# Kernel optimization log

Hardware: AMD Instinct MI355X
Metric: run time of the kernel (lower is better)

The kernel has to match this reference:

```python
import jax, jax.numpy as jnp
import numpy as np

B, L, D, F_, H = 64, 64, 512, 32, 512  # batch, seq_len, in_dim, fanout, hidden_dim


def setup_inputs() -> dict:
    key = jax.random.key(0)
    ks = jax.random.split(key, 8)
    x = jax.random.normal(ks[0], (B, L, D), dtype=jnp.float32)
    idx1 = jax.random.randint(ks[1], (B, F_), 0, L)          # hop-1 neighbor token ids
    idx2 = jax.random.randint(ks[2], (B, F_ * F_), 0, L)     # hop-2 neighbor token ids
    s_d = 1.0 / np.sqrt(D)
    s_h = 1.0 / np.sqrt(H)
    W_aggr0 = jax.random.normal(ks[3], (D, H), dtype=jnp.float32) * s_d
    b_aggr0 = jnp.zeros((H,), dtype=jnp.float32)
    W_self0 = jax.random.normal(ks[4], (D, H), dtype=jnp.float32) * s_d
    W_aggr1 = jax.random.normal(ks[5], (H, H), dtype=jnp.float32) * s_h
    b_aggr1 = jnp.zeros((H,), dtype=jnp.float32)
    W_self1 = jax.random.normal(ks[6], (H, H), dtype=jnp.float32) * s_h
    return {"x": x, "idx1": idx1, "idx2": idx2,
            "W_aggr0": W_aggr0, "b_aggr0": b_aggr0, "W_self0": W_self0,
            "W_aggr1": W_aggr1, "b_aggr1": b_aggr1, "W_self1": W_self1}


def _sage_gcn(src, nbr, W_aggr, b_aggr, W_self):
    # src: [B, N, d]; nbr: [B, N, F, d]. mean-aggregate + linear, sum with self-transform.
    aggr = jnp.mean(nbr, axis=2) @ W_aggr + b_aggr          # NeighborAggregator('mean')
    return src @ W_self + aggr                               # aggr_hidden_method='sum'


def reference(x, idx1, idx2, W_aggr0, b_aggr0, W_self0, W_aggr1, b_aggr1, W_self1):
    # Gather sampled node features per aspect (level 0 = aspect node itself, index 0).
    f0 = x[:, :1, :]                                               # [B, 1, D]
    f1 = jnp.take_along_axis(x, idx1[:, :, None], axis=1)          # [B, F, D]
    f2 = jnp.take_along_axis(x, idx2[:, :, None], axis=1)          # [B, F*F, D]

    # Layer 0 (shared gcn[0] weights across hops), leaky_relu activation.
    h0 = jax.nn.leaky_relu(_sage_gcn(f0, f1[:, None, :, :], W_aggr0, b_aggr0, W_self0))          # [B,1,H]
    h1 = jax.nn.leaky_relu(_sage_gcn(f1, f2.reshape(B, F_, F_, D), W_aggr0, b_aggr0, W_self0))   # [B,F,H]

    # Layer 1 (gcn[-1], activation=None).
    out = _sage_gcn(h0, h1[:, None, :, :], W_aggr1, b_aggr1, W_self1)                             # [B,1,H]
    return out
```

## Files before the change

kernel.cpp:

```cpp
#include <hip/hip_runtime.h>
#include <hip/hip_bf16.h>

#define B_ 64
#define L_ 64
#define D_ 512
#define F_ 32
#define H_ 512
#define M_ROWS 2048
#define M2 2112
#define KA 1024

typedef __attribute__((ext_vector_type(8))) short bf16x8;
typedef __attribute__((ext_vector_type(4))) float f32x4;

__device__ __forceinline__ float leaky(float v) { return v > 0.0f ? v : 0.01f * v; }

__device__ __forceinline__ unsigned short f2bf(float v) {
  unsigned int b = __float_as_uint(v);
  unsigned int r = b + 0x7FFF + ((b >> 16) & 1);
  return (unsigned short)(r >> 16);
}
__device__ __forceinline__ float bf2f(unsigned short h) {
  return __uint_as_float(((unsigned int)h) << 16);
}
__device__ __forceinline__ void cvt_store4(unsigned short* ph, unsigned short* pl, float4 v) {
  ushort4 h, l;
  h.x = f2bf(v.x); l.x = f2bf(v.x - bf2f(h.x));
  h.y = f2bf(v.y); l.y = f2bf(v.y - bf2f(h.y));
  h.z = f2bf(v.z); l.z = f2bf(v.z - bf2f(h.z));
  h.w = f2bf(v.w); l.w = f2bf(v.w - bf2f(h.w));
  *(ushort4*)ph = h;
  *(ushort4*)pl = l;
}

#define GLOAD16(GP, LP)                                              \
  __builtin_amdgcn_global_load_lds(                                  \
      (const __attribute__((address_space(1))) unsigned int*)(GP),   \
      (__attribute__((address_space(3))) unsigned int*)(LP), 16, 0, 0)

__global__ __launch_bounds__(256) void prep(
    const float* __restrict__ x, const int* __restrict__ idx1,
    const int* __restrict__ idx2,
    const float* __restrict__ Ws0, const float* __restrict__ Wa0,
    const float* __restrict__ Ws1, const float* __restrict__ Wa1,
    unsigned short* __restrict__ Xhi, unsigned short* __restrict__ Xlo,
    unsigned short* __restrict__ Mh, unsigned short* __restrict__ Ml,
    unsigned short* __restrict__ W0thi, unsigned short* __restrict__ W0tlo,
    unsigned short* __restrict__ W1thi, unsigned short* __restrict__ W1tlo) {
  __shared__ __align__(16) char smem[33024];
  const int blk = blockIdx.x;
  const int t = threadIdx.x;

  if (blk < 64) {
    const int b = blk;
    const float* src = x + (size_t)b * (L_ * D_);
    unsigned short* dh = Xhi + (size_t)b * (L_ * D_);
    unsigned short* dl = Xlo + (size_t)b * (L_ * D_);
#pragma unroll 4
    for (int i = 0; i < 32; ++i) {
      const int f4 = t + 256 * i;
      const float4 v = *(const float4*)(src + (size_t)f4 * 4);
      cvt_store4(dh + (size_t)f4 * 4, dl + (size_t)f4 * 4, v);
    }
  } else if (blk < 320) {
    const int q = blk - 64;
    const int k0 = (q & 15) * 64;
    const int n0 = ((q >> 4) & 7) * 64;
    const int cat = q >> 7;
    float (*lt)[72] = (float(*)[72])smem;
    const float* src = (cat == 0)
        ? (k0 < 512 ? Ws0 + (size_t)k0 * H_ : Wa0 + (size_t)(k0 - 512) * H_)
        : (k0 < 512 ? Ws1 + (size_t)k0 * H_ : Wa1 + (size_t)(k0 - 512) * H_);
    unsigned short* dhi = (cat == 0) ? W0thi : W1thi;
    unsigned short* dlo = (cat == 0) ? W0tlo : W1tlo;
#pragma unroll
    for (int i = 0; i < 4; ++i) {
      const int idx4 = t + 256 * i;
      const int kl = idx4 >> 4;
      const int n4 = (idx4 & 15) * 4;
      *(float4*)&lt[kl][n4] = *(const float4*)(src + (size_t)kl * H_ + n0 + n4);
    }
    __syncthreads();
#pragma unroll
    for (int i = 0; i < 4; ++i) {
      const int idx4 = t + 256 * i;
      const int nl = idx4 >> 4;
      const int k4 = (idx4 & 15) * 4;
      ushort4 h, l;
      const float v0 = lt[k4 + 0][nl], v1 = lt[k4 + 1][nl];
      const float v2 = lt[k4 + 2][nl], v3 = lt[k4 + 3][nl];
      h.x = f2bf(v0); l.x = f2bf(v0 - bf2f(h.x));
      h.y = f2bf(v1); l.y = f2bf(v1 - bf2f(h.y));
      h.z = f2bf(v2); l.z = f2bf(v2 - bf2f(h.z));
      h.w = f2bf(v3); l.w = f2bf(v3 - bf2f(h.w));
      *(ushort4*)(dhi + (size_t)(n0 + nl) * KA + k0 + k4) = h;
      *(ushort4*)(dlo + (size_t)(n0 + nl) * KA + k0 + k4) = l;
    }
  } else {
    const int q = blk - 320;
    const int b = q >> 2;
    const int nt0 = (q & 3) * 2;
    unsigned int* cnt = (unsigned int*)smem;
    unsigned short* Cm = (unsigned short*)(smem + 8448);
    unsigned short* XTh = (unsigned short*)(smem + 14592);
    unsigned short* XTl = XTh + 64 * 72;
    const int lane = t & 63;
    const int w = t >> 6;
    const int lr = lane & 15;
    const int kb8 = (lane >> 4) * 8;

#pragma unroll
    for (int i = 0; i < 9; ++i) { const int p = t + 256 * i; if (p < 2112) cnt[p] = 0u; }
#pragma unroll
    for (int i = 0; i < 12; ++i) Cm[t + 256 * i] = 0;
    __syncthreads();
#pragma unroll
    for (int i = 0; i < 4; ++i) {
      const int j = t + 256 * i;
      atomicAdd(&cnt[(j >> 5) * 64 + idx2[(size_t)b * 1024 + j]], 1u);
    }
    if (t < 32) atomicAdd(&cnt[32 * 64 + idx1[b * F_ + t]], 1u);
    __syncthreads();
#pragma unroll
    for (int i = 0; i < 9; ++i) {
      const int p = t + 256 * i;
      if (p < 2112) Cm[p] = f2bf((float)cnt[p] * 0.03125f);
    }
    __syncthreads();
    bf16x8 Af[3][2];
#pragma unroll
    for (int mi = 0; mi < 3; ++mi)
#pragma unroll
      for (int kt = 0; kt < 2; ++kt)
        Af[mi][kt] = *(const bf16x8*)&Cm[(mi * 16 + lr) * 64 + kt * 32 + kb8];

#pragma unroll
    for (int tt = 0; tt < 2; ++tt) {
      const int nbase = (nt0 + tt) * 64;
#pragma unroll
      for (int i = 0; i < 4; ++i) {
        const int f4 = t + 256 * i;
        const int l = f4 >> 4;
        const int c4 = (f4 & 15) * 4;
        const float4 v = *(const float4*)(x + (size_t)b * (L_ * D_) + (size_t)l * D_ + nbase + c4);
        unsigned short h;
        h = f2bf(v.x); XTh[(c4 + 0) * 72 + l] = h; XTl[(c4 + 0) * 72 + l] = f2bf(v.x - bf2f(h));
        h = f2bf(v.y); XTh[(c4 + 1) * 72 + l] = h; XTl[(c4 + 1) * 72 + l] = f2bf(v.y - bf2f(h));
        h = f2bf(v.z); XTh[(c4 + 2) * 72 + l] = h; XTl[(c4 + 2) * 72 + l] = f2bf(v.z - bf2f(h));
        h = f2bf(v.w); XTh[(c4 + 3) * 72 + l] = h; XTl[(c4 + 3) * 72 + l] = f2bf(v.w - bf2f(h));
      }
      __syncthreads();
      f32x4 acc[3] = {};
#pragma unroll
      for (int kt = 0; kt < 2; ++kt) {
        const bf16x8 Bh = *(const bf16x8*)&XTh[(w * 16 + lr) * 72 + kt * 32 + kb8];
        const bf16x8 Bl = *(const bf16x8*)&XTl[(w * 16 + lr) * 72 + kt * 32 + kb8];
#pragma unroll
        for (int mi = 0; mi < 3; ++mi) {
          acc[mi] = __builtin_amdgcn_mfma_f32_16x16x32_bf16(Af[mi][kt], Bh, acc[mi], 0, 0, 0);
          acc[mi] = __builtin_amdgcn_mfma_f32_16x16x32_bf16(Af[mi][kt], Bl, acc[mi], 0, 0, 0);
        }
      }
      const int col = nbase + w * 16 + lr;
#pragma unroll
      for (int mi = 0; mi < 3; ++mi)
#pragma unroll
        for (int r = 0; r < 4; ++r) {
          const int row48 = mi * 16 + (lane >> 4) * 4 + r;
          if (row48 > 32) continue;
          const size_t Mrow = (row48 < 32) ? (size_t)(b * F_ + row48) : (size_t)(M_ROWS + b);
          const float v = acc[mi][r];
          const unsigned short h = f2bf(v);
          Mh[Mrow * 512 + col] = h;
          Ml[Mrow * 512 + col] = f2bf(v - bf2f(h));
        }
      __syncthreads();
    }
  }
}

__global__ __launch_bounds__(256) void gemm1(
    const unsigned short* __restrict__ Xhi, const unsigned short* __restrict__ Xlo,
    const unsigned short* __restrict__ Mh, const unsigned short* __restrict__ Ml,
    const unsigned short* __restrict__ Wthi, const unsigned short* __restrict__ Wtlo,
    const int* __restrict__ idx1, const float* __restrict__ b0,
    unsigned short* __restrict__ Hhi, unsigned short* __restrict__ Hlo) {
  __shared__ unsigned short lds[24576];
  const int tid = threadIdx.x;
  const int lane = tid & 63;
  const int w = tid >> 6;
  const int wr = w >> 1, wc = w & 1;
  const int lr = lane & 15;
  const int kb = lane >> 4;
  const int swz = lr & 7;
  const int rsel = lane >> 3;
  const int cbs = ((lane & 7) ^ rsel) * 8;

  const int o = blockIdx.x;
  const int s = (o & 7) * 66 + (o >> 3);
  const int bmi = s >> 4;
  const int bni = s & 15;
  const int bm = bmi * 64;
  const int bn = bni * 32;

  int xrow[8];
  if (w < 2) {
#pragma unroll
    for (int i = 0; i < 8; ++i) {
      const int R = bm + rsel + 8 * i;
      if (bmi < 32) xrow[i] = (R >> 5) * 64 + idx1[R];
      else          xrow[i] = (R - M_ROWS) * 64;
    }
  }
  const unsigned short* Xp = (w == 0) ? Xhi : Xlo;
  const unsigned short* Mp = (w == 0) ? Mh : Ml;
  const unsigned short* Wp = (w == 2) ? Wthi : Wtlo;
  const unsigned short* mbase = Mp + (size_t)(bm + rsel) * 512 + cbs;
  const unsigned short* wbase = Wp + (size_t)(bn + rsel) * KA + cbs;
  const int PB = (w == 0) ? 0 : (w == 1) ? 4096 : (w == 2) ? 8192 : 10240;

#define STAGE(KT, BUF)                                                        \
  {                                                                           \
    unsigned short* ldst = &lds[(BUF)*12288 + PB];                            \
    if (w < 2) {                                                              \
      if ((KT) < 8) {                                                         \
        const int co = (KT)*64 + cbs;                                         \
        _Pragma("unroll") for (int i = 0; i < 8; ++i)                         \
            GLOAD16(Xp + (size_t)xrow[i] * 512 + co, ldst + i * 512);         \
      } else {                                                                \
        const unsigned short* mb = mbase + ((KT)-8) * 64;                     \
        _Pragma("unroll") for (int i = 0; i < 8; ++i)                         \
            GLOAD16(mb + (size_t)i * 8 * 512, ldst + i * 512);                \
      }                                                                       \
    } else {                                                                  \
      const unsigned short* wb = wbase + (KT)*64;                             \
      _Pragma("unroll") for (int i = 0; i < 4; ++i)                           \
          GLOAD16(wb + (size_t)i * 8 * KA, ldst + i * 512);                   \
    }                                                                         \
  }

  f32x4 acc[2] = {};
  STAGE(0, 0);
  __syncthreads();

#define AFRAG(PL, ROW, CB) \
  (*(const bf16x8*)&lds[buf * 12288 + (PL)*4096 + (ROW)*64 + (((CB) ^ swz) * 8)])
#define BFRAG(PL, ROW, CB) \
  (*(const bf16x8*)&lds[buf * 12288 + 8192 + (PL)*2048 + (ROW)*64 + (((CB) ^ swz) * 8)])

  for (int kt = 0; kt < 16; ++kt) {
    const int buf = kt & 1;
    if (kt < 15) STAGE(kt + 1, buf ^ 1);
#pragma unroll
    for (int ks = 0; ks < 2; ++ks) {
      const int c = ks * 4 + kb;
      const bf16x8 Ah0 = AFRAG(0, wr * 32 + lr, c);
      const bf16x8 Ah1 = AFRAG(0, wr * 32 + 16 + lr, c);
      const bf16x8 Al0 = AFRAG(1, wr * 32 + lr, c);
      const bf16x8 Al1 = AFRAG(1, wr * 32 + 16 + lr, c);
      const bf16x8 Bh = BFRAG(0, wc * 16 + lr, c);
      const bf16x8 Bl = BFRAG(1, wc * 16 + lr, c);
      acc[0] = __builtin_amdgcn_mfma_f32_16x16x32_bf16(Ah0, Bh, acc[0], 0, 0, 0);
      acc[0] = __builtin_amdgcn_mfma_f32_16x16x32_bf16(Ah0, Bl, acc[0], 0, 0, 0);
      acc[0] = __builtin_amdgcn_mfma_f32_16x16x32_bf16(Al0, Bh, acc[0], 0, 0, 0);
      acc[1] = __builtin_amdgcn_mfma_f32_16x16x32_bf16(Ah1, Bh, acc[1], 0, 0, 0);
      acc[1] = __builtin_amdgcn_mfma_f32_16x16x32_bf16(Ah1, Bl, acc[1], 0, 0, 0);
      acc[1] = __builtin_amdgcn_mfma_f32_16x16x32_bf16(Al1, Bh, acc[1], 0, 0, 0);
    }
    __syncthreads();
  }
#undef AFRAG
#undef BFRAG
#undef STAGE

  const int col = bn + wc * 16 + lr;
  const float bias = b0[col];
  if (bmi < 32) {
    const int b = bmi * 2 + wr;
    float sum = 0.f;
#pragma unroll
    for (int mi = 0; mi < 2; ++mi)
#pragma unroll
      for (int r = 0; r < 4; ++r) sum += leaky(acc[mi][r] + bias);
    sum += __shfl_xor(sum, 16);
    sum += __shfl_xor(sum, 32);
    sum *= (1.0f / 32.0f);
    if (lane < 16) {
      const unsigned short h = f2bf(sum);
      Hhi[(size_t)b * KA + 512 + col] = h;
      Hlo[(size_t)b * KA + 512 + col] = f2bf(sum - bf2f(h));
    }
  } else {
#pragma unroll
    for (int mi = 0; mi < 2; ++mi)
#pragma unroll
      for (int r = 0; r < 4; ++r) {
        const int b = wr * 32 + mi * 16 + kb * 4 + r;
        const float v = leaky(acc[mi][r] + bias);
        const unsigned short h = f2bf(v);
        Hhi[(size_t)b * KA + col] = h;
        Hlo[(size_t)b * KA + col] = f2bf(v - bf2f(h));
      }
  }
}

__global__ __launch_bounds__(256) void gemm2(
    const unsigned short* __restrict__ Hhi, const unsigned short* __restrict__ Hlo,
    const unsigned short* __restrict__ Wthi, const unsigned short* __restrict__ Wtlo,
    float* __restrict__ part) {
  __shared__ float sacc[256][17];
  const int tid = threadIdx.x;
  const int w = tid >> 6;
  const int lane = tid & 63;
  const int lr = lane & 15;
  const int kb = lane >> 4;
  const int n0 = blockIdx.x * 16;
  const int kc = blockIdx.y * 128;

  f32x4 acc[4] = {};
  const int k = kc + w * 32 + kb * 8;
  const bf16x8 Bh = *(const bf16x8*)(Wthi + (size_t)(n0 + lr) * KA + k);
  const bf16x8 Bl = *(const bf16x8*)(Wtlo + (size_t)(n0 + lr) * KA + k);
#pragma unroll
  for (int mi = 0; mi < 4; ++mi) {
    const bf16x8 Ah = *(const bf16x8*)(Hhi + (size_t)(mi * 16 + lr) * KA + k);
    const bf16x8 Al = *(const bf16x8*)(Hlo + (size_t)(mi * 16 + lr) * KA + k);
    acc[mi] = __builtin_amdgcn_mfma_f32_16x16x32_bf16(Ah, Bh, acc[mi], 0, 0, 0);
    acc[mi] = __builtin_amdgcn_mfma_f32_16x16x32_bf16(Ah, Bl, acc[mi], 0, 0, 0);
    acc[mi] = __builtin_amdgcn_mfma_f32_16x16x32_bf16(Al, Bh, acc[mi], 0, 0, 0);
  }
#pragma unroll
  for (int mi = 0; mi < 4; ++mi)
#pragma unroll
    for (int r = 0; r < 4; ++r)
      sacc[((w * 4 + mi) * 4 + kb) * 4 + r][lr] = acc[mi][r];
  __syncthreads();

  const int lr2 = tid & 15;
  const int rg = tid >> 4;
  float* pp = part + (size_t)blockIdx.y * (B_ * H_);
#pragma unroll
  for (int q = 0; q < 4; ++q) {
    const int row = rg * 4 + q;
    const int mi = row >> 4, kb2 = (row >> 2) & 3, r = row & 3;
    float s = 0.f;
#pragma unroll
    for (int w2 = 0; w2 < 4; ++w2)
      s += sacc[((w2 * 4 + mi) * 4 + kb2) * 4 + r][lr2];
    pp[(size_t)row * H_ + n0 + lr2] = s;
  }
}

__global__ __launch_bounds__(256) void reduce_out(
    const float* __restrict__ part, const float* __restrict__ b1,
    float* __restrict__ out) {
  const int idx = blockIdx.x * 256 + threadIdx.x;
  const int c4 = (idx & 127) * 4;
  const size_t off = (size_t)(idx >> 7) * H_ + c4;
  float4 s = *(const float4*)(b1 + c4);
#pragma unroll
  for (int ky = 0; ky < 8; ++ky) {
    const float4 p = *(const float4*)(part + (size_t)ky * (B_ * H_) + off);
    s.x += p.x; s.y += p.y; s.z += p.z; s.w += p.w;
  }
  *(float4*)(out + off) = s;
}

extern "C" void kernel_launch(void* const* d_in, const int* in_sizes, int n_in,
                              void* d_out, int out_size, void* d_ws, size_t ws_size,
                              hipStream_t stream) {
  const float* x    = (const float*)d_in[0];
  const int*   idx1 = (const int*)d_in[1];
  const int*   idx2 = (const int*)d_in[2];
  const float* Wa0  = (const float*)d_in[3];
  const float* b0   = (const float*)d_in[4];
  const float* Ws0  = (const float*)d_in[5];
  const float* Wa1  = (const float*)d_in[6];
  const float* b1   = (const float*)d_in[7];
  const float* Ws1  = (const float*)d_in[8];
  float* out = (float*)d_out;

  unsigned short* wsu = (unsigned short*)d_ws;
  unsigned short* Xhi   = wsu;
  unsigned short* Xlo   = Xhi + (size_t)4096 * 512;
  unsigned short* Mh    = Xlo + (size_t)4096 * 512;
  unsigned short* Ml    = Mh + (size_t)M2 * 512;
  unsigned short* W0thi = Ml + (size_t)M2 * 512;
  unsigned short* W0tlo = W0thi + (size_t)H_ * KA;
  unsigned short* W1thi = W0tlo + (size_t)H_ * KA;
  unsigned short* W1tlo = W1thi + (size_t)H_ * KA;
  unsigned short* Hhi   = W1tlo + (size_t)H_ * KA;
  unsigned short* Hlo   = Hhi + (size_t)B_ * KA;
  float* part = (float*)(Hlo + (size_t)B_ * KA);

  prep<<<576, 256, 0, stream>>>(x, idx1, idx2, Ws0, Wa0, Ws1, Wa1,
                                Xhi, Xlo, Mh, Ml, W0thi, W0tlo, W1thi, W1tlo);
  gemm1<<<528, 256, 0, stream>>>(Xhi, Xlo, Mh, Ml, W0thi, W0tlo,
                                 idx1, b0, Hhi, Hlo);
  gemm2<<<dim3(32, 8), 256, 0, stream>>>(Hhi, Hlo, W1thi, W1tlo, part);
  reduce_out<<<32, 256, 0, stream>>>(part, b1, out);
}
```

Measured before the change: 40.64 us.

## Restructure gemm1: stage weights in LDS per half, stream A directly from global

```diff
diff --git a/kernel.cpp b/kernel.cpp
--- a/kernel.cpp
+++ b/kernel.cpp
@@ -185,16 +185,12 @@
     const unsigned short* __restrict__ Wthi, const unsigned short* __restrict__ Wtlo,
     const int* __restrict__ idx1, const float* __restrict__ b0,
     unsigned short* __restrict__ Hhi, unsigned short* __restrict__ Hlo) {
-  __shared__ unsigned short lds[24576];
+  __shared__ __align__(16) unsigned short lds[32768];
   const int tid = threadIdx.x;
   const int lane = tid & 63;
   const int w = tid >> 6;
-  const int wr = w >> 1, wc = w & 1;
   const int lr = lane & 15;
-  const int kb = lane >> 4;
-  const int swz = lr & 7;
-  const int rsel = lane >> 3;
-  const int cbs = ((lane & 7) ^ rsel) * 8;
+  const int kq = lane >> 4;
 
   const int o = blockIdx.x;
   const int s = (o & 7) * 66 + (o >> 3);
@@ -203,104 +199,96 @@
   const int bm = bmi * 64;
   const int bn = bni * 32;
 
-  int xrow[8];
-  if (w < 2) {
-#pragma unroll
-    for (int i = 0; i < 8; ++i) {
-      const int R = bm + rsel + 8 * i;
-      if (bmi < 32) xrow[i] = (R >> 5) * 64 + idx1[R];
-      else          xrow[i] = (R - M_ROWS) * 64;
-    }
-  }
-  const unsigned short* Xp = (w == 0) ? Xhi : Xlo;
-  const unsigned short* Mp = (w == 0) ? Mh : Ml;
-  const unsigned short* Wp = (w == 2) ? Wthi : Wtlo;
-  const unsigned short* mbase = Mp + (size_t)(bm + rsel) * 512 + cbs;
-  const unsigned short* wbase = Wp + (size_t)(bn + rsel) * KA + cbs;
-  const int PB = (w == 0) ? 0 : (w == 1) ? 4096 : (w == 2) ? 8192 : 10240;
-
-#define STAGE(KT, BUF)                                                        \
-  {                                                                           \
-    unsigned short* ldst = &lds[(BUF)*12288 + PB];                            \
-    if (w < 2) {                                                              \
-      if ((KT) < 8) {                                                         \
-        const int co = (KT)*64 + cbs;                                         \
-        _Pragma("unroll") for (int i = 0; i < 8; ++i)                         \
-            GLOAD16(Xp + (size_t)xrow[i] * 512 + co, ldst + i * 512);         \
-      } else {                                                                \
-        const unsigned short* mb = mbase + ((KT)-8) * 64;                     \
-        _Pragma("unroll") for (int i = 0; i < 8; ++i)                         \
-            GLOAD16(mb + (size_t)i * 8 * 512, ldst + i * 512);                \
-      }                                                                       \
-    } else {                                                                  \
-      const unsigned short* wb = wbase + (KT)*64;                             \
-      _Pragma("unroll") for (int i = 0; i < 4; ++i)                           \
-          GLOAD16(wb + (size_t)i * 8 * KA, ldst + i * 512);                   \
-    }                                                                         \
-  }
-
-  f32x4 acc[2] = {};
-  STAGE(0, 0);
-  __syncthreads();
-
-#define AFRAG(PL, ROW, CB) \
-  (*(const bf16x8*)&lds[buf * 12288 + (PL)*4096 + (ROW)*64 + (((CB) ^ swz) * 8)])
-#define BFRAG(PL, ROW, CB) \
-  (*(const bf16x8*)&lds[buf * 12288 + 8192 + (PL)*2048 + (ROW)*64 + (((CB) ^ swz) * 8)])
-
-  for (int kt = 0; kt < 16; ++kt) {
-    const int buf = kt & 1;
-    if (kt < 15) STAGE(kt + 1, buf ^ 1);
-#pragma unroll
-    for (int ks = 0; ks < 2; ++ks) {
-      const int c = ks * 4 + kb;
-      const bf16x8 Ah0 = AFRAG(0, wr * 32 + lr, c);
-      const bf16x8 Ah1 = AFRAG(0, wr * 32 + 16 + lr, c);
-      const bf16x8 Al0 = AFRAG(1, wr * 32 + lr, c);
-      const bf16x8 Al1 = AFRAG(1, wr * 32 + 16 + lr, c);
-      const bf16x8 Bh = BFRAG(0, wc * 16 + lr, c);
-      const bf16x8 Bl = BFRAG(1, wc * 16 + lr, c);
-      acc[0] = __builtin_amdgcn_mfma_f32_16x16x32_bf16(Ah0, Bh, acc[0], 0, 0, 0);
-      acc[0] = __builtin_amdgcn_mfma_f32_16x16x32_bf16(Ah0, Bl, acc[0], 0, 0, 0);
-      acc[0] = __builtin_amdgcn_mfma_f32_16x16x32_bf16(Al0, Bh, acc[0], 0, 0, 0);
-      acc[1] = __builtin_amdgcn_mfma_f32_16x16x32_bf16(Ah1, Bh, acc[1], 0, 0, 0);
-      acc[1] = __builtin_amdgcn_mfma_f32_16x16x32_bf16(Ah1, Bl, acc[1], 0, 0, 0);
-      acc[1] = __builtin_amdgcn_mfma_f32_16x16x32_bf16(Al1, Bh, acc[1], 0, 0, 0);
-    }
-    __syncthreads();
-  }
-#undef AFRAG
-#undef BFRAG
-#undef STAGE
-
-  const int col = bn + wc * 16 + lr;
-  const float bias = b0[col];
+  const int R = bm + w * 16 + lr;
+  const int xr = (bmi < 32) ? ((R >> 5) * 64 + idx1[R]) : ((R - M_ROWS) * 64);
+  const unsigned short* aXh = Xhi + (size_t)xr * 512 + kq * 8;
+  const unsigned short* aXl = Xlo + (size_t)xr * 512 + kq * 8;
+  const unsigned short* aMh = Mh + (size_t)R * 512 + kq * 8;
+  const unsigned short* aMl = Ml + (size_t)R * 512 + kq * 8;
+
+  f32x4 accHH[2] = {};
+  f32x4 accX[2] = {};
+
+  for (int c = 0; c < 2; ++c) {
+#pragma unroll
+    for (int i = 0; i < 16; ++i) {
+      const int slot = (w * 16 + i) * 64 + lane;
+      const int pl = slot >> 11;
+      const int row = (slot >> 6) & 31;
+      const int cb = slot & 63;
+      const unsigned short* gp = (pl ? Wtlo : Wthi) +
+          (size_t)(bn + row) * KA + c * 512 + ((cb ^ (row & 7)) * 8);
+      GLOAD16(gp, &lds[(w * 16 + i) * 512]);
+    }
+    __syncthreads();
+
+    const unsigned short* ah = (c == 0) ? aXh : aMh;
+    const unsigned short* al = (c == 0) ? aXl : aMl;
+
+    bf16x8 Ah = *(const bf16x8*)(ah);
+    bf16x8 Al = *(const bf16x8*)(al);
+#pragma unroll
+    for (int ks = 0; ks < 16; ++ks) {
+      const int nk = (ks + 1) & 15;
+      const bf16x8 AhN = *(const bf16x8*)(ah + nk * 32);
+      const bf16x8 AlN = *(const bf16x8*)(al + nk * 32);
+#pragma unroll
+      for (int nf = 0; nf < 2; ++nf) {
+        const int row = nf * 16 + lr;
+        const int cbX = (ks * 4 + kq) ^ (row & 7);
+        const bf16x8 Bh = *(const bf16x8*)&lds[row * 512 + cbX * 8];
+        const bf16x8 Bl = *(const bf16x8*)&lds[16384 + row * 512 + cbX * 8];
+        accHH[nf] = __builtin_amdgcn_mfma_f32_16x16x32_bf16(Ah, Bh, accHH[nf], 0, 0, 0);
+        accX[nf]  = __builtin_amdgcn_mfma_f32_16x16x32_bf16(Ah, Bl, accX[nf], 0, 0, 0);
+        accX[nf]  = __builtin_amdgcn_mfma_f32_16x16x32_bf16(Al, Bh, accX[nf], 0, 0, 0);
+      }
+      Ah = AhN;
+      Al = AlN;
+    }
+    __syncthreads();
+  }
+
+  f32x4 acc[2];
+  acc[0] = accHH[0] + accX[0];
+  acc[1] = accHH[1] + accX[1];
+
   if (bmi < 32) {
-    const int b = bmi * 2 + wr;
-    float sum = 0.f;
-#pragma unroll
-    for (int mi = 0; mi < 2; ++mi)
-#pragma unroll
-      for (int r = 0; r < 4; ++r) sum += leaky(acc[mi][r] + bias);
-    sum += __shfl_xor(sum, 16);
-    sum += __shfl_xor(sum, 32);
-    sum *= (1.0f / 32.0f);
-    if (lane < 16) {
-      const unsigned short h = f2bf(sum);
-      Hhi[(size_t)b * KA + 512 + col] = h;
-      Hlo[(size_t)b * KA + 512 + col] = f2bf(sum - bf2f(h));
+    float* P = (float*)lds;
+#pragma unroll
+    for (int nf = 0; nf < 2; ++nf) {
+      const int col = bn + nf * 16 + lr;
+      const float bias = b0[col];
+      float sv = 0.f;
+#pragma unroll
+      for (int r = 0; r < 4; ++r) sv += leaky(acc[nf][r] + bias);
+      sv += __shfl_xor(sv, 16);
+      sv += __shfl_xor(sv, 32);
+      if (lane < 16) P[w * 32 + nf * 16 + lane] = sv;
+    }
+    __syncthreads();
+    if (tid < 64) {
+      const int half = tid >> 5;
+      const int col = tid & 31;
+      const int b = bmi * 2 + half;
+      const float sv = (P[(half * 2) * 32 + col] + P[(half * 2 + 1) * 32 + col]) * (1.0f / 32.0f);
+      const unsigned short h = f2bf(sv);
+      Hhi[(size_t)b * KA + 512 + bn + col] = h;
+      Hlo[(size_t)b * KA + 512 + bn + col] = f2bf(sv - bf2f(h));
     }
   } else {
 #pragma unroll
-    for (int mi = 0; mi < 2; ++mi)
+    for (int nf = 0; nf < 2; ++nf) {
+      const int col = bn + nf * 16 + lr;
+      const float bias = b0[col];
 #pragma unroll
       for (int r = 0; r < 4; ++r) {
-        const int b = wr * 32 + mi * 16 + kb * 4 + r;
-        const float v = leaky(acc[mi][r] + bias);
+        const int bb = w * 16 + kq * 4 + r;
+        const float v = leaky(acc[nf][r] + bias);
         const unsigned short h = f2bf(v);
-        Hhi[(size_t)b * KA + col] = h;
-        Hlo[(size_t)b * KA + col] = f2bf(v - bf2f(h));
+        Hhi[(size_t)bb * KA + col] = h;
+        Hlo[(size_t)bb * KA + col] = f2bf(v - bf2f(h));
       }
+    }
   }
 }
 
@@ -343,11 +331,11 @@
   for (int q = 0; q < 4; ++q) {
     const int row = rg * 4 + q;
     const int mi = row >> 4, kb2 = (row >> 2) & 3, r = row & 3;
-    float s = 0.f;
+    float sv = 0.f;
 #pragma unroll
     for (int w2 = 0; w2 < 4; ++w2)
-      s += sacc[((w2 * 4 + mi) * 4 + kb2) * 4 + r][lr2];
-    pp[(size_t)row * H_ + n0 + lr2] = s;
+      sv += sacc[((w2 * 4 + mi) * 4 + kb2) * 4 + r][lr2];
+    pp[(size_t)row * H_ + n0 + lr2] = sv;
   }
 }
 
```

After: 56.86 us. 1.4x slower.

## Fuse split-K reduction and bias into single-block-per-column gemm2

Applied to the files above, without the earlier changes.

```diff
diff --git a/kernel.cpp b/kernel.cpp
--- a/kernel.cpp
+++ b/kernel.cpp
@@ -304,66 +304,51 @@
   }
 }
 
-__global__ __launch_bounds__(256) void gemm2(
+__global__ __launch_bounds__(512) void gemm2f(
     const unsigned short* __restrict__ Hhi, const unsigned short* __restrict__ Hlo,
     const unsigned short* __restrict__ Wthi, const unsigned short* __restrict__ Wtlo,
-    float* __restrict__ part) {
-  __shared__ float sacc[256][17];
+    const float* __restrict__ b1, float* __restrict__ out) {
+  __shared__ float sacc[8][1088];
   const int tid = threadIdx.x;
   const int w = tid >> 6;
   const int lane = tid & 63;
   const int lr = lane & 15;
   const int kb = lane >> 4;
   const int n0 = blockIdx.x * 16;
-  const int kc = blockIdx.y * 128;
+  const int kc = w * 128;
 
   f32x4 acc[4] = {};
-  const int k = kc + w * 32 + kb * 8;
-  const bf16x8 Bh = *(const bf16x8*)(Wthi + (size_t)(n0 + lr) * KA + k);
-  const bf16x8 Bl = *(const bf16x8*)(Wtlo + (size_t)(n0 + lr) * KA + k);
-#pragma unroll
-  for (int mi = 0; mi < 4; ++mi) {
-    const bf16x8 Ah = *(const bf16x8*)(Hhi + (size_t)(mi * 16 + lr) * KA + k);
-    const bf16x8 Al = *(const bf16x8*)(Hlo + (size_t)(mi * 16 + lr) * KA + k);
-    acc[mi] = __builtin_amdgcn_mfma_f32_16x16x32_bf16(Ah, Bh, acc[mi], 0, 0, 0);
-    acc[mi] = __builtin_amdgcn_mfma_f32_16x16x32_bf16(Ah, Bl, acc[mi], 0, 0, 0);
-    acc[mi] = __builtin_amdgcn_mfma_f32_16x16x32_bf16(Al, Bh, acc[mi], 0, 0, 0);
+#pragma unroll
+  for (int ks = 0; ks < 4; ++ks) {
+    const int k = kc + ks * 32 + kb * 8;
+    const bf16x8 Bh = *(const bf16x8*)(Wthi + (size_t)(n0 + lr) * KA + k);
+    const bf16x8 Bl = *(const bf16x8*)(Wtlo + (size_t)(n0 + lr) * KA + k);
+#pragma unroll
+    for (int mi = 0; mi < 4; ++mi) {
+      const bf16x8 Ah = *(const bf16x8*)(Hhi + (size_t)(mi * 16 + lr) * KA + k);
+      const bf16x8 Al = *(const bf16x8*)(Hlo + (size_t)(mi * 16 + lr) * KA + k);
+      acc[mi] = __builtin_amdgcn_mfma_f32_16x16x32_bf16(Ah, Bh, acc[mi], 0, 0, 0);
+      acc[mi] = __builtin_amdgcn_mfma_f32_16x16x32_bf16(Ah, Bl, acc[mi], 0, 0, 0);
+      acc[mi] = __builtin_amdgcn_mfma_f32_16x16x32_bf16(Al, Bh, acc[mi], 0, 0, 0);
+    }
   }
 #pragma unroll
   for (int mi = 0; mi < 4; ++mi)
 #pragma unroll
     for (int r = 0; r < 4; ++r)
-      sacc[((w * 4 + mi) * 4 + kb) * 4 + r][lr] = acc[mi][r];
+      sacc[w][(mi * 16 + kb * 4 + r) * 17 + lr] = acc[mi][r];
   __syncthreads();
 
-  const int lr2 = tid & 15;
-  const int rg = tid >> 4;
-  float* pp = part + (size_t)blockIdx.y * (B_ * H_);
-#pragma unroll
-  for (int q = 0; q < 4; ++q) {
-    const int row = rg * 4 + q;
-    const int mi = row >> 4, kb2 = (row >> 2) & 3, r = row & 3;
-    float s = 0.f;
-#pragma unroll
-    for (int w2 = 0; w2 < 4; ++w2)
-      s += sacc[((w2 * 4 + mi) * 4 + kb2) * 4 + r][lr2];
-    pp[(size_t)row * H_ + n0 + lr2] = s;
-  }
-}
-
-__global__ __launch_bounds__(256) void reduce_out(
-    const float* __restrict__ part, const float* __restrict__ b1,
-    float* __restrict__ out) {
-  const int idx = blockIdx.x * 256 + threadIdx.x;
-  const int c4 = (idx & 127) * 4;
-  const size_t off = (size_t)(idx >> 7) * H_ + c4;
-  float4 s = *(const float4*)(b1 + c4);
-#pragma unroll
-  for (int ky = 0; ky < 8; ++ky) {
-    const float4 p = *(const float4*)(part + (size_t)ky * (B_ * H_) + off);
-    s.x += p.x; s.y += p.y; s.z += p.z; s.w += p.w;
-  }
-  *(float4*)(out + off) = s;
+#pragma unroll
+  for (int q = 0; q < 2; ++q) {
+    const int oid = tid * 2 + q;
+    const int row = oid >> 4;
+    const int col = oid & 15;
+    float sv = b1[n0 + col];
+#pragma unroll
+    for (int w2 = 0; w2 < 8; ++w2) sv += sacc[w2][row * 17 + col];
+    out[(size_t)row * H_ + n0 + col] = sv;
+  }
 }
 
 extern "C" void kernel_launch(void* const* d_in, const int* in_sizes, int n_in,
@@ -391,12 +376,10 @@
   unsigned short* W1tlo = W1thi + (size_t)H_ * KA;
   unsigned short* Hhi   = W1tlo + (size_t)H_ * KA;
   unsigned short* Hlo   = Hhi + (size_t)B_ * KA;
-  float* part = (float*)(Hlo + (size_t)B_ * KA);
 
   prep<<<576, 256, 0, stream>>>(x, idx1, idx2, Ws0, Wa0, Ws1, Wa1,
                                 Xhi, Xlo, Mh, Ml, W0thi, W0tlo, W1thi, W1tlo);
   gemm1<<<528, 256, 0, stream>>>(Xhi, Xlo, Mh, Ml, W0thi, W0tlo,
                                  idx1, b0, Hhi, Hlo);
-  gemm2<<<dim3(32, 8), 256, 0, stream>>>(Hhi, Hlo, W1thi, W1tlo, part);
-  reduce_out<<<32, 256, 0, stream>>>(part, b1, out);
-}
+  gemm2f<<<32, 512, 0, stream>>>(Hhi, Hlo, W1thi, W1tlo, b1, out);
+}
```

Result: slower. 46.53 us (+14.5%).
